# Performance work log

Measured on AMD Instinct MI355X. Metric: run time of the kernel, lower is better.

Reference implementation:

```python
import jax, jax.numpy as jnp
import numpy as np

B, T, H, I, OUT = 128, 1440, 512, 2, 1
TAU, ALPHA = 6.0, 0.1


def setup_inputs() -> dict:
    key = jax.random.key(0)
    ks = jax.random.split(key, 8)
    xs = jax.random.normal(ks[0], (B, T), dtype=jnp.float32)
    # sparse 0/1 observation mask (channel 2); channel 1 unused by forward
    mask = (jax.random.uniform(ks[1], (B, T)) < 0.05).astype(jnp.float32)
    inp = jnp.stack([xs, jnp.zeros((B, T), jnp.float32), mask], axis=1)[..., None]  # [B,3,T,1]
    s = 1.0 / np.sqrt(H)
    u = lambda k, shp: jax.random.uniform(k, shp, minval=-s, maxval=s, dtype=jnp.float32)
    return {
        "input": inp,
        "w_ih": u(ks[2], (3 * H, I)),
        "w_hh": u(ks[3], (3 * H, H)),
        "b_ih": u(ks[4], (3 * H,)),
        "b_hh": u(ks[5], (3 * H,)),
        "w_fc": u(ks[6], (OUT, H)),
        "b_fc": u(ks[7], (OUT,)),
    }


def belief_fill(x, mask, half_tau):
    # Vectorized equivalent of the per-batch / per-observed-index Python loop:
    # each position takes the value of the next observed index if within half_tau
    # else the previous observed index if within half_tau, else stays unchanged.
    Ts = x.shape[1]
    t = jnp.arange(Ts)[None, :]
    obs = mask == 1
    p = jax.lax.cummax(jnp.where(obs, t, -1), axis=1)                       # prev observed idx or -1
    n = jax.lax.cummin(jnp.where(obs, t, Ts)[:, ::-1], axis=1)[:, ::-1]      # next observed idx or Ts
    xp = jnp.take_along_axis(x, jnp.clip(p, 0, Ts - 1), axis=1)
    xn = jnp.take_along_axis(x, jnp.clip(n, 0, Ts - 1), axis=1)
    use_n = (n < Ts) & (t >= n - half_tau)
    use_p = (p >= 0) & (t <= p + half_tau)
    return jnp.where(use_n, xn, jnp.where(use_p, xp, x))


def _forward(inp, w_ih, w_hh, b_ih, b_hh, w_fc, b_fc):
    xs = inp[:, 0, :, 0]      # [B,T]
    masks = inp[:, 2, :, 0]   # [B,T]
    xs = jnp.where(jnp.isnan(xs), -1.0, xs)
    # tau update: old_weight is ones(3H, I)
    grads = jnp.mean(w_ih - 1.0)
    tau_new = TAU + grads * ALPHA
    trigger = (tau_new >= 1.0) & (tau_new != TAU)
    half_tau = jnp.round(tau_new / 2.0)
    xs = jnp.where(trigger, belief_fill(xs, masks, half_tau), xs)
    gru_in = jnp.stack((xs, masks), axis=2)  # [B,T,2]
    # precompute input projections once (the only input-dependent GEMM)
    gi = jnp.einsum('bti,gi->btg', gru_in, w_ih) + b_ih  # [B,T,3H]

    def step(h, gi_t):
        gh = h @ w_hh.T + b_hh
        r = jax.nn.sigmoid(gi_t[:, :H] + gh[:, :H])
        z = jax.nn.sigmoid(gi_t[:, H:2 * H] + gh[:, H:2 * H])
        ng = jnp.tanh(gi_t[:, 2 * H:] + r * gh[:, 2 * H:])
        h = (1.0 - z) * ng + z * h
        return h, None

    h0 = jnp.zeros((inp.shape[0], H), gi.dtype)
    h_last, _ = jax.lax.scan(step, h0, jnp.swapaxes(gi, 0, 1))
    return h_last @ w_fc.T + b_fc  # [B, OUT]


def reference(input, w_ih, w_hh, b_ih, b_hh, w_fc, b_fc):
    return _forward(input, w_ih, w_hh, b_ih, b_hh, w_fc, b_fc)
```

## Files before the change

### kernel.cpp

```cpp
#include <hip/hip_runtime.h>
#include <math.h>

#define BN   128
#define TN   1440
#define HN   512
#define GBn  8
#define BSn  16
#define GCn  32
#define HCn  16
#define WST  536

using f16 = _Float16;
typedef f16   f16x8 __attribute__((ext_vector_type(8)));
typedef float f32x4 __attribute__((ext_vector_type(4)));
typedef unsigned int       uint32;
typedef unsigned long long u64;

#define OFF_SCAL 1024
#define OFF_HBUF 2048
#define OFF_XSF  (2048 + 2 * BN * HN * 4)

__global__ void k_prep(const float* __restrict__ w_ih, float* __restrict__ scal) {
    __shared__ float ssum[4];
    float s = 0.0f;
    for (int i = threadIdx.x; i < 3 * HN * 2; i += 256) s += w_ih[i];
    for (int o = 32; o >= 1; o >>= 1) s += __shfl_down(s, o, 64);
    if ((threadIdx.x & 63) == 0) ssum[threadIdx.x >> 6] = s;
    __syncthreads();
    if (threadIdx.x == 0) {
        float tot = ssum[0] + ssum[1] + ssum[2] + ssum[3];
        float grads = tot / 3072.0f - 1.0f;
        float tau_new = 6.0f + grads * 0.1f;
        bool trig = (tau_new >= 1.0f) && (tau_new != 6.0f);
        scal[0] = rintf(tau_new * 0.5f);
        scal[1] = trig ? 1.0f : 0.0f;
    }
}

__global__ void k_fill(const float* __restrict__ inp, const float* __restrict__ scal,
                       float* __restrict__ xsf) {
    const int b = blockIdx.x;
    const int lane = threadIdx.x;
    const float ht = scal[0];
    const bool trig = scal[1] != 0.0f;
    const float* xrow = inp + (size_t)b * 3 * TN;
    const float* mrow = xrow + 2 * TN;
    const int CH = 23;
    const int start = lane * CH;

    if (!trig) {
        for (int i = 0; i < CH; ++i) {
            int t = start + i;
            if (t < TN) { float x = xrow[t]; if (x != x) x = -1.0f; xsf[(size_t)b * TN + t] = x; }
        }
        return;
    }
    int pm = -1;
#pragma unroll
    for (int i = 0; i < CH; ++i) { int t = start + i; if (t < TN && mrow[t] == 1.0f) pm = t; }
    int incl = pm;
    for (int o = 1; o < 64; o <<= 1) { int v = __shfl_up(incl, o, 64); if (lane >= o) incl = max(incl, v); }
    int pexcl = __shfl_up(incl, 1, 64); if (lane == 0) pexcl = -1;
    int nm = TN;
#pragma unroll
    for (int i = CH - 1; i >= 0; --i) { int t = start + i; if (t < TN && mrow[t] == 1.0f) nm = t; }
    int incl2 = nm;
    for (int o = 1; o < 64; o <<= 1) { int v = __shfl_down(incl2, o, 64); if (lane + o < 64) incl2 = min(incl2, v); }
    int nexcl = __shfl_down(incl2, 1, 64); if (lane == 63) nexcl = TN;
    int narr[23];
    int runn = nexcl;
#pragma unroll
    for (int i = CH - 1; i >= 0; --i) {
        int t = start + i;
        if (t < TN) { if (mrow[t] == 1.0f) runn = t; narr[i] = runn; } else narr[i] = TN;
    }
    int runp = pexcl;
#pragma unroll
    for (int i = 0; i < CH; ++i) {
        int t = start + i;
        if (t >= TN) break;
        float x = xrow[t]; if (x != x) x = -1.0f;
        if (mrow[t] == 1.0f) runp = t;
        int pv = runp, nv = narr[i];
        int pc = min(max(pv, 0), TN - 1), nc = min(max(nv, 0), TN - 1);
        float xp = xrow[pc]; if (xp != xp) xp = -1.0f;
        float xn = xrow[nc]; if (xn != xn) xn = -1.0f;
        bool use_n = (nv < TN) && ((float)t >= (float)nv - ht);
        bool use_p = (pv >= 0) && ((float)t <= (float)pv + ht);
        float o = use_n ? xn : (use_p ? xp : x);
        xsf[(size_t)b * TN + t] = o;
    }
}

__global__ __launch_bounds__(256, 1) void k_gru(
    const float* __restrict__ inp, const float* __restrict__ w_ih,
    const float* __restrict__ w_hh, const float* __restrict__ b_ih,
    const float* __restrict__ b_hh, const float* __restrict__ w_fc,
    const float* __restrict__ b_fc, const float* __restrict__ xsf,
    uint32* __restrict__ hbufP, int* __restrict__ flags, float* __restrict__ out) {
    __shared__ __align__(16) f16 sHhi[BSn * WST];
    __shared__ __align__(16) f16 sHlo[BSn * WST];
    __shared__ float sGh[3][BSn][HCn + 1];
    __shared__ float sWi0[48], sWi1[48], sBias[48];

    const int tid = threadIdx.x;
    const int gb = blockIdx.x & 7;
    const int gc = blockIdx.x >> 3;
    const int lane = tid & 63;
    const int wv   = tid >> 6;
    const int bs   = tid >> 4;
    const int j    = tid & 15;
    const int bglob = gb * BSn + bs;
    const int pcol  = gc * HCn + j;
    const int frow = lane & 15;
    const int kgrp = lane >> 4;

    if (tid < 48) {
        int gate = tid >> 4, jj = tid & 15;
        int grow = gate * HN + gc * HCn + jj;
        sWi0[tid]  = w_ih[grow * 2 + 0];
        sWi1[tid]  = w_ih[grow * 2 + 1];
        sBias[tid] = b_ih[grow] + b_hh[grow];
    }

    f16x8 bfh[16], bfl[16];
    if (wv < 3) {
        const float* wrow = w_hh + (size_t)(wv * HN + gc * HCn + frow) * HN;
#pragma unroll
        for (int c = 0; c < 16; ++c) {
            const int k0 = (c * 4 + kgrp) * 8;
#pragma unroll
            for (int u = 0; u < 8; ++u) {
                float w = wrow[k0 + u];
                f16 hi = (f16)w;
                bfh[c][u] = hi;
                bfl[c][u] = (f16)((w - (float)hi) * 2048.0f);
            }
        }
    }
    __syncthreads();

    int* myflags = flags + gb * GCn;
    const f16x8* pAhi = (const f16x8*)(sHhi + frow * WST);
    const f16x8* pAlo = (const f16x8*)(sHlo + frow * WST);
    float h = 0.0f;

    for (int t = 0; t < TN; ++t) {
        float xsv = xsf[(size_t)bglob * TN + t];
        float mkv = inp[((size_t)bglob * 3 + 2) * TN + t];
        if (lane < GCn) {
            while (__hip_atomic_load(&myflags[lane], __ATOMIC_RELAXED, __HIP_MEMORY_SCOPE_AGENT) < t) {}
        }
        {
            const uint32* src = hbufP + ((size_t)(t & 1) * BN + gb * BSn) * HN;
            u64 hv[16];
#pragma unroll
            for (int i = 0; i < 16; ++i)
                hv[i] = __hip_atomic_load((const u64*)(src + (size_t)i * HN) + tid,
                                          __ATOMIC_RELAXED, __HIP_MEMORY_SCOPE_AGENT);
#pragma unroll
            for (int i = 0; i < 16; ++i) {
                uint32 d0 = (uint32)hv[i], d1 = (uint32)(hv[i] >> 32);
                ((uint32*)(sHhi + i * WST))[tid] = __builtin_amdgcn_perm(d1, d0, 0x05040100u);
                ((uint32*)(sHlo + i * WST))[tid] = __builtin_amdgcn_perm(d1, d0, 0x07060302u);
            }
        }
        __syncthreads();
        if (wv < 3) {
            f32x4 ah0 = {0.f,0.f,0.f,0.f}, ah1 = {0.f,0.f,0.f,0.f};
            f32x4 al0 = {0.f,0.f,0.f,0.f}, al1 = {0.f,0.f,0.f,0.f};
            f32x4 bl0 = {0.f,0.f,0.f,0.f}, bl1 = {0.f,0.f,0.f,0.f};
#pragma unroll
            for (int c = 0; c < 16; c += 2) {
                f16x8 ha = pAhi[c * 4 + kgrp];
                f16x8 la = pAlo[c * 4 + kgrp];
                f16x8 hb = pAhi[(c + 1) * 4 + kgrp];
                f16x8 lb = pAlo[(c + 1) * 4 + kgrp];
                ah0 = __builtin_amdgcn_mfma_f32_16x16x32_f16(ha, bfh[c],     ah0, 0, 0, 0);
                ah1 = __builtin_amdgcn_mfma_f32_16x16x32_f16(hb, bfh[c + 1], ah1, 0, 0, 0);
                al0 = __builtin_amdgcn_mfma_f32_16x16x32_f16(ha, bfl[c],     al0, 0, 0, 0);
                al1 = __builtin_amdgcn_mfma_f32_16x16x32_f16(hb, bfl[c + 1], al1, 0, 0, 0);
                bl0 = __builtin_amdgcn_mfma_f32_16x16x32_f16(la, bfh[c],     bl0, 0, 0, 0);
                bl1 = __builtin_amdgcn_mfma_f32_16x16x32_f16(lb, bfh[c + 1], bl1, 0, 0, 0);
            }
#pragma unroll
            for (int r = 0; r < 4; ++r)
                sGh[wv][kgrp * 4 + r][frow] =
                    (ah0[r] + ah1[r]) + (al0[r] + al1[r] + bl0[r] + bl1[r]) * (1.0f / 2048.0f);
        }
        __syncthreads();
        {
            float ghr = sGh[0][bs][j], ghz = sGh[1][bs][j], ghn = sGh[2][bs][j];
            float gir = xsv * sWi0[j]      + mkv * sWi1[j]      + sBias[j];
            float giz = xsv * sWi0[16 + j] + mkv * sWi1[16 + j] + sBias[16 + j];
            float gin = xsv * sWi0[32 + j] + mkv * sWi1[32 + j] + sBias[32 + j];
            float rg = __fdividef(1.0f, 1.0f + __expf(-(gir + ghr)));
            float zg = __fdividef(1.0f, 1.0f + __expf(-(giz + ghz)));
            float xt = gin + rg * ghn;
            float ng = __fdividef(2.0f, 1.0f + __expf(-2.0f * xt)) - 1.0f;
            h = (1.0f - zg) * ng + zg * h;
            f16 hi = (f16)h;
            f16 lo = (f16)((h - (float)hi) * 2048.0f);
            uint32 pk = (uint32)__builtin_bit_cast(unsigned short, hi)
                      | ((uint32)__builtin_bit_cast(unsigned short, lo) << 16);
            __hip_atomic_store(&hbufP[((size_t)((t + 1) & 1) * BN + bglob) * HN + pcol], pk,
                               __ATOMIC_RELAXED, __HIP_MEMORY_SCOPE_AGENT);
        }
        __syncthreads();
        if (tid == 0)
            __hip_atomic_store(&myflags[gc], t + 1, __ATOMIC_RELAXED, __HIP_MEMORY_SCOPE_AGENT);
    }
    float part = h * w_fc[pcol];
#pragma unroll
    for (int o = 1; o < 16; o <<= 1) part += __shfl_xor(part, o, 64);
    if (j == 0) {
        if (gc == 0) part += b_fc[0];
        atomicAdd(&out[bglob], part);
    }
}

extern "C" void kernel_launch(void* const* d_in, const int* in_sizes, int n_in,
                              void* d_out, int out_size, void* d_ws, size_t ws_size,
                              hipStream_t stream) {
    const float* inp  = (const float*)d_in[0];
    const float* w_ih = (const float*)d_in[1];
    const float* w_hh = (const float*)d_in[2];
    const float* b_ih = (const float*)d_in[3];
    const float* b_hh = (const float*)d_in[4];
    const float* w_fc = (const float*)d_in[5];
    const float* b_fc = (const float*)d_in[6];
    float* out = (float*)d_out;
    char* ws = (char*)d_ws;
    int*    flags = (int*)ws;
    float*  scal  = (float*)(ws + OFF_SCAL);
    uint32* hbufP = (uint32*)(ws + OFF_HBUF);
    float*  xsf   = (float*)(ws + OFF_XSF);

    hipMemsetAsync(ws, 0, OFF_HBUF + BN * HN * 4, stream);
    hipMemsetAsync(d_out, 0, BN * sizeof(float), stream);
    k_prep<<<1, 256, 0, stream>>>(w_ih, scal);
    k_fill<<<BN, 64, 0, stream>>>(inp, scal, xsf);
    k_gru<<<GBn * GCn, 256, 0, stream>>>(inp, w_ih, w_hh, b_ih, b_hh, w_fc, b_fc,
                                         xsf, hbufP, flags, out);
}
```

Before: 3.837 ms.

## Interleave two batch groups per block to hide cross-block hidden-state exchange latency

Each block now handles two batch groups (A and B) and alternates between them within each timestep. While one group's matmul and gate update run, the block waits on flags and loads the other group's hidden state from global memory. This is meant to overlap the inter-block synchronization and global-load latency with compute. Block count halves from 256 to 128, so each block does twice the MFMA work and fewer CUs are busy.

```diff
diff --git a/kernel.cpp b/kernel.cpp
--- a/kernel.cpp
+++ b/kernel.cpp
@@ -6,6 +6,7 @@
 #define HN   512
 #define GBn  8
 #define BSn  16
+#define GPn  4
 #define GCn  32
 #define HCn  16
 #define WST  536
@@ -104,13 +105,15 @@
     __shared__ float sWi0[48], sWi1[48], sBias[48];
 
     const int tid = threadIdx.x;
-    const int gb = blockIdx.x & 7;
-    const int gc = blockIdx.x >> 3;
+    const int gp = blockIdx.x & 3;
+    const int gc = blockIdx.x >> 2;
+    const int gbA = gp * 2, gbB = gp * 2 + 1;
     const int lane = tid & 63;
     const int wv   = tid >> 6;
     const int bs   = tid >> 4;
     const int j    = tid & 15;
-    const int bglob = gb * BSn + bs;
+    const int bglobA = gbA * BSn + bs;
+    const int bglobB = gbB * BSn + bs;
     const int pcol  = gc * HCn + j;
     const int frow = lane & 15;
     const int kgrp = lane >> 4;
@@ -140,32 +143,45 @@
     }
     __syncthreads();
 
-    int* myflags = flags + gb * GCn;
+    int* flagsA = flags + gbA * GCn;
+    int* flagsB = flags + gbB * GCn;
     const f16x8* pAhi = (const f16x8*)(sHhi + frow * WST);
     const f16x8* pAlo = (const f16x8*)(sHlo + frow * WST);
-    float h = 0.0f;
+    float hA = 0.0f, hB = 0.0f;
+    u64 hvA[16], hvB[16];
+
+    {
+        const uint32* srcA = hbufP + (size_t)gbA * BSn * HN;
+#pragma unroll
+        for (int i = 0; i < 16; ++i)
+            hvA[i] = __hip_atomic_load((const u64*)(srcA + (size_t)i * HN) + tid,
+                                       __ATOMIC_RELAXED, __HIP_MEMORY_SCOPE_AGENT);
+    }
 
     for (int t = 0; t < TN; ++t) {
-        float xsv = xsf[(size_t)bglob * TN + t];
-        float mkv = inp[((size_t)bglob * 3 + 2) * TN + t];
+        float xsvA = xsf[(size_t)bglobA * TN + t];
+        float mkvA = inp[((size_t)bglobA * 3 + 2) * TN + t];
+        float xsvB = xsf[(size_t)bglobB * TN + t];
+        float mkvB = inp[((size_t)bglobB * 3 + 2) * TN + t];
+
+#pragma unroll
+        for (int i = 0; i < 16; ++i) {
+            uint32 d0 = (uint32)hvA[i], d1 = (uint32)(hvA[i] >> 32);
+            ((uint32*)(sHhi + i * WST))[tid] = __builtin_amdgcn_perm(d1, d0, 0x05040100u);
+            ((uint32*)(sHlo + i * WST))[tid] = __builtin_amdgcn_perm(d1, d0, 0x07060302u);
+        }
+        __syncthreads();
         if (lane < GCn) {
-            while (__hip_atomic_load(&myflags[lane], __ATOMIC_RELAXED, __HIP_MEMORY_SCOPE_AGENT) < t) {}
+            while (__hip_atomic_load(&flagsB[lane], __ATOMIC_RELAXED,
+                                     __HIP_MEMORY_SCOPE_AGENT) < t) {}
         }
         {
-            const uint32* src = hbufP + ((size_t)(t & 1) * BN + gb * BSn) * HN;
-            u64 hv[16];
+            const uint32* srcB = hbufP + ((size_t)(t & 1) * BN + gbB * BSn) * HN;
 #pragma unroll
             for (int i = 0; i < 16; ++i)
-                hv[i] = __hip_atomic_load((const u64*)(src + (size_t)i * HN) + tid,
-                                          __ATOMIC_RELAXED, __HIP_MEMORY_SCOPE_AGENT);
-#pragma unroll
-            for (int i = 0; i < 16; ++i) {
-                uint32 d0 = (uint32)hv[i], d1 = (uint32)(hv[i] >> 32);
-                ((uint32*)(sHhi + i * WST))[tid] = __builtin_amdgcn_perm(d1, d0, 0x05040100u);
-                ((uint32*)(sHlo + i * WST))[tid] = __builtin_amdgcn_perm(d1, d0, 0x07060302u);
-            }
-        }
-        __syncthreads();
+                hvB[i] = __hip_atomic_load((const u64*)(srcB + (size_t)i * HN) + tid,
+                                           __ATOMIC_RELAXED, __HIP_MEMORY_SCOPE_AGENT);
+        }
         if (wv < 3) {
             f32x4 ah0 = {0.f,0.f,0.f,0.f}, ah1 = {0.f,0.f,0.f,0.f};
             f32x4 al0 = {0.f,0.f,0.f,0.f}, al1 = {0.f,0.f,0.f,0.f};
@@ -191,31 +207,98 @@
         __syncthreads();
         {
             float ghr = sGh[0][bs][j], ghz = sGh[1][bs][j], ghn = sGh[2][bs][j];
-            float gir = xsv * sWi0[j]      + mkv * sWi1[j]      + sBias[j];
-            float giz = xsv * sWi0[16 + j] + mkv * sWi1[16 + j] + sBias[16 + j];
-            float gin = xsv * sWi0[32 + j] + mkv * sWi1[32 + j] + sBias[32 + j];
+            float gir = xsvA * sWi0[j]      + mkvA * sWi1[j]      + sBias[j];
+            float giz = xsvA * sWi0[16 + j] + mkvA * sWi1[16 + j] + sBias[16 + j];
+            float gin = xsvA * sWi0[32 + j] + mkvA * sWi1[32 + j] + sBias[32 + j];
             float rg = __fdividef(1.0f, 1.0f + __expf(-(gir + ghr)));
             float zg = __fdividef(1.0f, 1.0f + __expf(-(giz + ghz)));
             float xt = gin + rg * ghn;
             float ng = __fdividef(2.0f, 1.0f + __expf(-2.0f * xt)) - 1.0f;
-            h = (1.0f - zg) * ng + zg * h;
-            f16 hi = (f16)h;
-            f16 lo = (f16)((h - (float)hi) * 2048.0f);
+            hA = (1.0f - zg) * ng + zg * hA;
+            f16 hi = (f16)hA;
+            f16 lo = (f16)((hA - (float)hi) * 2048.0f);
             uint32 pk = (uint32)__builtin_bit_cast(unsigned short, hi)
                       | ((uint32)__builtin_bit_cast(unsigned short, lo) << 16);
-            __hip_atomic_store(&hbufP[((size_t)((t + 1) & 1) * BN + bglob) * HN + pcol], pk,
+            __hip_atomic_store(&hbufP[((size_t)((t + 1) & 1) * BN + bglobA) * HN + pcol], pk,
                                __ATOMIC_RELAXED, __HIP_MEMORY_SCOPE_AGENT);
         }
+#pragma unroll
+        for (int i = 0; i < 16; ++i) {
+            uint32 d0 = (uint32)hvB[i], d1 = (uint32)(hvB[i] >> 32);
+            ((uint32*)(sHhi + i * WST))[tid] = __builtin_amdgcn_perm(d1, d0, 0x05040100u);
+            ((uint32*)(sHlo + i * WST))[tid] = __builtin_amdgcn_perm(d1, d0, 0x07060302u);
+        }
         __syncthreads();
         if (tid == 0)
-            __hip_atomic_store(&myflags[gc], t + 1, __ATOMIC_RELAXED, __HIP_MEMORY_SCOPE_AGENT);
-    }
-    float part = h * w_fc[pcol];
-#pragma unroll
-    for (int o = 1; o < 16; o <<= 1) part += __shfl_xor(part, o, 64);
+            __hip_atomic_store(&flagsA[gc], t + 1, __ATOMIC_RELAXED, __HIP_MEMORY_SCOPE_AGENT);
+
+        if (wv < 3) {
+            f32x4 ah0 = {0.f,0.f,0.f,0.f}, ah1 = {0.f,0.f,0.f,0.f};
+            f32x4 al0 = {0.f,0.f,0.f,0.f}, al1 = {0.f,0.f,0.f,0.f};
+            f32x4 bl0 = {0.f,0.f,0.f,0.f}, bl1 = {0.f,0.f,0.f,0.f};
+#pragma unroll
+            for (int c = 0; c < 16; c += 2) {
+                f16x8 ha = pAhi[c * 4 + kgrp];
+                f16x8 la = pAlo[c * 4 + kgrp];
+                f16x8 hb = pAhi[(c + 1) * 4 + kgrp];
+                f16x8 lb = pAlo[(c + 1) * 4 + kgrp];
+                ah0 = __builtin_amdgcn_mfma_f32_16x16x32_f16(ha, bfh[c],     ah0, 0, 0, 0);
+                ah1 = __builtin_amdgcn_mfma_f32_16x16x32_f16(hb, bfh[c + 1], ah1, 0, 0, 0);
+                al0 = __builtin_amdgcn_mfma_f32_16x16x32_f16(ha, bfl[c],     al0, 0, 0, 0);
+                al1 = __builtin_amdgcn_mfma_f32_16x16x32_f16(hb, bfl[c + 1], al1, 0, 0, 0);
+                bl0 = __builtin_amdgcn_mfma_f32_16x16x32_f16(la, bfh[c],     bl0, 0, 0, 0);
+                bl1 = __builtin_amdgcn_mfma_f32_16x16x32_f16(lb, bfh[c + 1], bl1, 0, 0, 0);
+            }
+#pragma unroll
+            for (int r = 0; r < 4; ++r)
+                sGh[wv][kgrp * 4 + r][frow] =
+                    (ah0[r] + ah1[r]) + (al0[r] + al1[r] + bl0[r] + bl1[r]) * (1.0f / 2048.0f);
+        }
+        __syncthreads();
+        if (t + 1 < TN) {
+            if (lane < GCn) {
+                while (__hip_atomic_load(&flagsA[lane], __ATOMIC_RELAXED,
+                                         __HIP_MEMORY_SCOPE_AGENT) < t + 1) {}
+            }
+            const uint32* srcA = hbufP + ((size_t)((t + 1) & 1) * BN + gbA * BSn) * HN;
+#pragma unroll
+            for (int i = 0; i < 16; ++i)
+                hvA[i] = __hip_atomic_load((const u64*)(srcA + (size_t)i * HN) + tid,
+                                           __ATOMIC_RELAXED, __HIP_MEMORY_SCOPE_AGENT);
+        }
+        {
+            float ghr = sGh[0][bs][j], ghz = sGh[1][bs][j], ghn = sGh[2][bs][j];
+            float gir = xsvB * sWi0[j]      + mkvB * sWi1[j]      + sBias[j];
+            float giz = xsvB * sWi0[16 + j] + mkvB * sWi1[16 + j] + sBias[16 + j];
+            float gin = xsvB * sWi0[32 + j] + mkvB * sWi1[32 + j] + sBias[32 + j];
+            float rg = __fdividef(1.0f, 1.0f + __expf(-(gir + ghr)));
+            float zg = __fdividef(1.0f, 1.0f + __expf(-(giz + ghz)));
+            float xt = gin + rg * ghn;
+            float ng = __fdividef(2.0f, 1.0f + __expf(-2.0f * xt)) - 1.0f;
+            hB = (1.0f - zg) * ng + zg * hB;
+            f16 hi = (f16)hB;
+            f16 lo = (f16)((hB - (float)hi) * 2048.0f);
+            uint32 pk = (uint32)__builtin_bit_cast(unsigned short, hi)
+                      | ((uint32)__builtin_bit_cast(unsigned short, lo) << 16);
+            __hip_atomic_store(&hbufP[((size_t)((t + 1) & 1) * BN + bglobB) * HN + pcol], pk,
+                               __ATOMIC_RELAXED, __HIP_MEMORY_SCOPE_AGENT);
+        }
+        __syncthreads();
+        if (tid == 0)
+            __hip_atomic_store(&flagsB[gc], t + 1, __ATOMIC_RELAXED, __HIP_MEMORY_SCOPE_AGENT);
+    }
+
+    float wfc = w_fc[pcol];
+    float partA = hA * wfc, partB = hB * wfc;
+#pragma unroll
+    for (int o = 1; o < 16; o <<= 1) {
+        partA += __shfl_xor(partA, o, 64);
+        partB += __shfl_xor(partB, o, 64);
+    }
     if (j == 0) {
-        if (gc == 0) part += b_fc[0];
-        atomicAdd(&out[bglob], part);
+        if (gc == 0) { partA += b_fc[0]; partB += b_fc[0]; }
+        atomicAdd(&out[bglobA], partA);
+        atomicAdd(&out[bglobB], partB);
     }
 }
 
@@ -240,6 +323,6 @@
     hipMemsetAsync(d_out, 0, BN * sizeof(float), stream);
     k_prep<<<1, 256, 0, stream>>>(w_ih, scal);
     k_fill<<<BN, 64, 0, stream>>>(inp, scal, xsf);
-    k_gru<<<GBn * GCn, 256, 0, stream>>>(inp, w_ih, w_hh, b_ih, b_hh, w_fc, b_fc,
+    k_gru<<<GPn * GCn, 256, 0, stream>>>(inp, w_ih, w_hh, b_ih, b_hh, w_fc, b_fc,
                                          xsf, hbufP, flags, out);
 }
```

After: 5.705 ms. 48.7% more time.
